# Kernel optimization log

Hardware: AMD Instinct MI355X
Metric: run time of the kernel (lower is better)

Reference implementation:

```python
import jax, jax.numpy as jnp
import numpy as np

# ---- static config (from module __init__ defaults) ----
INPUT_DIM = 3
NUM_LEVELS = 16
LEVEL_DIM = 2
SCALE = 2.0
BASE_RES = 16
LOG2_T = 19
MAX_T = 2 ** LOG2_T
NUM_FREQS = 6
N_POINTS = 2_000_000
PRIMES = np.array([1, 2654435761, 805459861], dtype=np.uint32)  # Instant-NGP spatial hash primes
CORNERS = np.array([[i, j, k] for i in (0, 1) for j in (0, 1) for k in (0, 1)], dtype=np.int32)  # [8,3]

RES = [int(np.floor(BASE_RES * SCALE ** l)) for l in range(NUM_LEVELS)]
SIZES = [min(MAX_T, (r + 1) ** 3) for r in RES]  # dense if the full grid fits in the hashmap
OFFSETS = np.concatenate([[0], np.cumsum(SIZES)]).astype(np.int64)
TOTAL = int(OFFSETS[-1])  # 7,131,219 rows


def setup_inputs() -> dict:
    key = jax.random.key(0)
    k1, k2 = jax.random.split(key)
    x = jax.random.uniform(k1, (N_POINTS, INPUT_DIM), dtype=jnp.float32)  # points in [0,1]^3
    # hash-grid features init U(-1e-4, 1e-4) as in Instant-NGP
    table = (jax.random.uniform(k2, (TOTAL, LEVEL_DIM), dtype=jnp.float32) * 2.0 - 1.0) * 1e-4
    return {"x": x, "table": table}


def _level_interp(x, table_l, res, size):
    """Trilinear hash-grid interpolation at one level. x:[N,3] in [0,1]."""
    pos = x * jnp.float32(res)            # [N,3]
    p0f = jnp.floor(pos)
    frac = pos - p0f                      # [N,3]
    p0 = p0f.astype(jnp.int32)
    corners = jnp.clip(p0[:, None, :] + CORNERS[None], 0, res)  # [N,8,3], grid has res+1 verts
    if (res + 1) ** 3 <= MAX_T:
        # dense stride indexing
        r1 = res + 1
        idx = corners[..., 0] + corners[..., 1] * r1 + corners[..., 2] * (r1 * r1)
    else:
        c = corners.astype(jnp.uint32)
        h = (c[..., 0] * jnp.uint32(int(PRIMES[0]))
             ^ c[..., 1] * jnp.uint32(int(PRIMES[1]))
             ^ c[..., 2] * jnp.uint32(int(PRIMES[2])))
        idx = (h % jnp.uint32(size)).astype(jnp.int32)
    vals = table_l[idx]                   # [N,8,level_dim] gather
    # trilinear weights: prod over dims of (frac if corner==1 else 1-frac)
    w = jnp.where(CORNERS[None] == 1, frac[:, None, :], 1.0 - frac[:, None, :]).prod(-1)  # [N,8]
    return jnp.einsum('nc,ncd->nd', w, vals)  # [N,level_dim]


def _hash_encode(x, table):
    feats = [
        _level_interp(x, table[int(OFFSETS[l]):int(OFFSETS[l + 1])], RES[l], SIZES[l])
        for l in range(NUM_LEVELS)
    ]
    return jnp.concatenate(feats, axis=-1)  # [N, num_levels*level_dim]


def _pos_encode(x):
    coeffs = jnp.float32(2.0) ** jnp.arange(NUM_FREQS, dtype=jnp.float32)  # log_sampling
    xc = x[:, None, :] * coeffs[None, :, None]           # [N,F,3]
    sc = jnp.stack([jnp.sin(xc), jnp.cos(xc)], axis=2)   # [N,F,2,3] -> order: per-freq sin(3) then cos(3)
    return jnp.concatenate([x, sc.reshape(x.shape[0], 2 * NUM_FREQS * INPUT_DIM)], axis=-1)


def reference(x, table):
    hash_feat = _hash_encode(x, table)   # [N,32]
    freq_feat = _pos_encode(x)           # [N,39]
    return jnp.concatenate([hash_feat, freq_feat], axis=-1)  # [N,71]
```

## Files before the change

kernel.cpp:

```cpp
#include <hip/hip_runtime.h>

typedef float f4 __attribute__((ext_vector_type(4)));

#define BLK 128
#define NLEV 16
#define NHASH 13
#define HSIZE 524288
#define HMASK 524287u
#define KOFF3 315475
#define CONV_BLOCKS ((NHASH * HSIZE) / 256)

__constant__ int kOff[NLEV] = {0, 4913, 40850, 315475, 839763, 1364051, 1888339,
                               2412627, 2936915, 3461203, 3985491, 4509779,
                               5034067, 5558355, 6082643, 6606931};

__global__ __launch_bounds__(256)
void prep_kernel(const float* __restrict__ xs, const float2* __restrict__ tab,
                 unsigned* __restrict__ tbf, f4* __restrict__ xs4, int n)
{
    const int b = blockIdx.x;
    if (b < CONV_BLOCKS) {
        const int i = b * 256 + threadIdx.x;
        float2 v = tab[KOFF3 + i];
        tbf[i] = (__float_as_uint(v.x) >> 16) | (__float_as_uint(v.y) & 0xFFFF0000u);
    } else {
        const int i = (b - CONV_BLOCKS) * 256 + threadIdx.x;
        if (i < n) {
            f4 p;
            p.x = xs[3 * i + 0];
            p.y = xs[3 * i + 1];
            p.z = xs[3 * i + 2];
            p.w = 0.f;
            __builtin_nontemporal_store(p, &xs4[i]);
        }
    }
}

__global__ __launch_bounds__(256)
void levels_kernel(const f4* __restrict__ xs4, const unsigned* __restrict__ tbf,
                   unsigned* __restrict__ scratch, int n)
{
    const int lev = blockIdx.y;
    const int i0  = blockIdx.x * 512 + threadIdx.x;
    const int res = 16 << (3 + lev);
    const float fres = (float)res;
    const unsigned* __restrict__ tl = tbf + (size_t)lev * HSIZE;

    unsigned hx[2], hc[2][4];
    float rx[2], ry[2], rz[2];
    bool valid[2];

    #pragma unroll
    for (int p = 0; p < 2; ++p) {
        const int i = i0 + p * 256;
        valid[p] = (i < n);
        f4 pt = {0.f, 0.f, 0.f, 0.f};
        if (valid[p]) pt = __builtin_nontemporal_load(&xs4[i]);
        float posx = pt.x * fres, posy = pt.y * fres, posz = pt.z * fres;
        float fxf = floorf(posx), fyf = floorf(posy), fzf = floorf(posz);
        rx[p] = posx - fxf; ry[p] = posy - fyf; rz[p] = posz - fzf;
        unsigned x  = (unsigned)(int)fxf;
        unsigned y0 = (unsigned)(int)fyf * 2654435761u, y1 = y0 + 2654435761u;
        unsigned z0 = (unsigned)(int)fzf * 805459861u,  z1 = z0 + 805459861u;
        hx[p] = x;
        hc[p][0] = y0 ^ z0; hc[p][1] = y0 ^ z1; hc[p][2] = y1 ^ z0; hc[p][3] = y1 ^ z1;
    }

    unsigned va[2][4], vb[2][4];
    #pragma unroll
    for (int p = 0; p < 2; ++p) {
        #pragma unroll
        for (int c = 0; c < 4; ++c) {
            unsigned ia = (hx[p] ^ hc[p][c]) & HMASK;
            uint2 q = *(const uint2*)(tl + (ia & ~1u));
            va[p][c] = (ia & 1u) ? q.y : q.x;
            vb[p][c] = (ia & 1u) ? q.x : q.y;
        }
    }
    #pragma unroll
    for (int p = 0; p < 2; ++p) {
        if (hx[p] & 1u) {
            unsigned x1 = hx[p] + 1u;
            #pragma unroll
            for (int c = 0; c < 4; ++c)
                vb[p][c] = tl[(x1 ^ hc[p][c]) & HMASK];
        }
    }

    #pragma unroll
    for (int p = 0; p < 2; ++p) {
        if (!valid[p]) continue;
        float wx1 = rx[p], wx0 = 1.f - wx1;
        float wy1 = ry[p], wy0 = 1.f - wy1;
        float wz1 = rz[p], wz0 = 1.f - wz1;
        float wc[4] = {wy0 * wz0, wy0 * wz1, wy1 * wz0, wy1 * wz1};
        float f0 = 0.f, f1 = 0.f;
        #pragma unroll
        for (int c = 0; c < 4; ++c) {
            float a0 = __uint_as_float(va[p][c] << 16);
            float a1 = __uint_as_float(va[p][c] & 0xFFFF0000u);
            float b0 = __uint_as_float(vb[p][c] << 16);
            float b1 = __uint_as_float(vb[p][c] & 0xFFFF0000u);
            f0 += wc[c] * (wx0 * a0 + wx1 * b0);
            f1 += wc[c] * (wx0 * a1 + wx1 * b1);
        }
        unsigned packed = (__float_as_uint(f0) >> 16) | (__float_as_uint(f1) & 0xFFFF0000u);
        __builtin_nontemporal_store(packed, &scratch[(size_t)lev * n + (i0 + p * 256)]);
    }
}

__global__ __launch_bounds__(256)
void levels_f32_kernel(const float* __restrict__ xs, const float2* __restrict__ tab,
                       unsigned* __restrict__ scratch, int n)
{
    const int lev = blockIdx.y;
    const int i   = blockIdx.x * 256 + threadIdx.x;
    if (i >= n) return;
    const int res = 16 << (3 + lev);
    const float2* __restrict__ tl = tab + kOff[3 + lev];

    const float px = __builtin_nontemporal_load(&xs[3 * i + 0]);
    const float py = __builtin_nontemporal_load(&xs[3 * i + 1]);
    const float pz = __builtin_nontemporal_load(&xs[3 * i + 2]);

    const float fres = (float)res;
    float posx = px * fres, posy = py * fres, posz = pz * fres;
    float fxf = floorf(posx), fyf = floorf(posy), fzf = floorf(posz);
    float rx = posx - fxf, ry = posy - fyf, rz = posz - fzf;

    unsigned hx  = (unsigned)(int)fxf;
    unsigned hy0 = (unsigned)(int)fyf * 2654435761u, hy1 = hy0 + 2654435761u;
    unsigned hz0 = (unsigned)(int)fzf * 805459861u,  hz1 = hz0 + 805459861u;
    unsigned h00 = hy0 ^ hz0, h01 = hy0 ^ hz1, h10 = hy1 ^ hz0, h11 = hy1 ^ hz1;

    unsigned hx1 = hx + 1u;
    float2 v000 = tl[(hx ^ h00) & HMASK], v100 = tl[(hx1 ^ h00) & HMASK];
    float2 v001 = tl[(hx ^ h01) & HMASK], v101 = tl[(hx1 ^ h01) & HMASK];
    float2 v010 = tl[(hx ^ h10) & HMASK], v110 = tl[(hx1 ^ h10) & HMASK];
    float2 v011 = tl[(hx ^ h11) & HMASK], v111 = tl[(hx1 ^ h11) & HMASK];

    float wx1 = rx, wx0 = 1.f - rx;
    float wy1 = ry, wy0 = 1.f - ry;
    float wz1 = rz, wz0 = 1.f - rz;

    float f0, f1, w;
    w = wx0 * wy0 * wz0; f0  = w * v000.x; f1  = w * v000.y;
    w = wx0 * wy0 * wz1; f0 += w * v001.x; f1 += w * v001.y;
    w = wx0 * wy1 * wz0; f0 += w * v010.x; f1 += w * v010.y;
    w = wx0 * wy1 * wz1; f0 += w * v011.x; f1 += w * v011.y;
    w = wx1 * wy0 * wz0; f0 += w * v100.x; f1 += w * v100.y;
    w = wx1 * wy0 * wz1; f0 += w * v101.x; f1 += w * v101.y;
    w = wx1 * wy1 * wz0; f0 += w * v110.x; f1 += w * v110.y;
    w = wx1 * wy1 * wz1; f0 += w * v111.x; f1 += w * v111.y;

    unsigned packed = (__float_as_uint(f0) >> 16) | (__float_as_uint(f1) & 0xFFFF0000u);
    __builtin_nontemporal_store(packed, &scratch[(size_t)lev * n + i]);
}

__global__ __launch_bounds__(BLK)
void final_kernel(const f4* __restrict__ xs4, const float* __restrict__ table,
                  const unsigned* __restrict__ scratch, float* __restrict__ out, int n)
{
    __shared__ float sbuf[BLK * 71];
    const int tid  = threadIdx.x;
    const int base = blockIdx.x * BLK;
    const int pi   = base + tid;
    const bool val = (pi < n);

    unsigned sc[NHASH];
    if (val) {
        #pragma unroll
        for (int h = 0; h < NHASH; ++h)
            sc[h] = __builtin_nontemporal_load(&scratch[(size_t)h * n + pi]);
    }

    f4 pt = {0.f, 0.f, 0.f, 0.f};
    if (val) pt = __builtin_nontemporal_load(&xs4[pi]);
    const float px = pt.x, py = pt.y, pz = pt.z;

    float* srow = sbuf + tid * 71;
    const float2* __restrict__ tab = (const float2*)table;

    #pragma unroll
    for (int l = 0; l < 3; ++l) {
        const int res = 16 << l;
        const float2* __restrict__ tl = tab + kOff[l];
        const float fres = (float)res;

        float posx = px * fres, posy = py * fres, posz = pz * fres;
        float fxf = floorf(posx), fyf = floorf(posy), fzf = floorf(posz);
        float rx = posx - fxf, ry = posy - fyf, rz = posz - fzf;

        const unsigned r1 = (unsigned)(res + 1);
        const unsigned r2 = r1 * r1;
        unsigned x0 = (unsigned)(int)fxf;
        unsigned by0 = (unsigned)(int)fyf * r1; unsigned by1 = by0 + r1;
        unsigned cz0 = (unsigned)(int)fzf * r2; unsigned cz1 = cz0 + r2;

        float2 v000, v001, v010, v011, v100, v101, v110, v111;
        #define PAIRD(B, VA, VB) { \
            unsigned i0 = x0 + (B); \
            if ((i0 & 1u) == 0u) { f4 q = *(const f4*)(tl + i0); \
                VA.x = q.x; VA.y = q.y; VB.x = q.z; VB.y = q.w; } \
            else { VA = tl[i0]; VB = tl[i0 + 1u]; } }
        PAIRD(by0 + cz0, v000, v100)
        PAIRD(by0 + cz1, v001, v101)
        PAIRD(by1 + cz0, v010, v110)
        PAIRD(by1 + cz1, v011, v111)
        #undef PAIRD

        float wx1 = rx, wx0 = 1.f - rx;
        float wy1 = ry, wy0 = 1.f - ry;
        float wz1 = rz, wz0 = 1.f - rz;

        float f0, f1, w;
        w = wx0 * wy0 * wz0; f0  = w * v000.x; f1  = w * v000.y;
        w = wx0 * wy0 * wz1; f0 += w * v001.x; f1 += w * v001.y;
        w = wx0 * wy1 * wz0; f0 += w * v010.x; f1 += w * v010.y;
        w = wx0 * wy1 * wz1; f0 += w * v011.x; f1 += w * v011.y;
        w = wx1 * wy0 * wz0; f0 += w * v100.x; f1 += w * v100.y;
        w = wx1 * wy0 * wz1; f0 += w * v101.x; f1 += w * v101.y;
        w = wx1 * wy1 * wz0; f0 += w * v110.x; f1 += w * v110.y;
        w = wx1 * wy1 * wz1; f0 += w * v111.x; f1 += w * v111.y;

        srow[2 * l]     = f0;
        srow[2 * l + 1] = f1;
    }

    #pragma unroll
    for (int h = 0; h < NHASH; ++h) {
        srow[6 + 2 * h] = __uint_as_float(sc[h] << 16);
        srow[7 + 2 * h] = __uint_as_float(sc[h] & 0xFFFF0000u);
    }

    srow[32] = px; srow[33] = py; srow[34] = pz;
    float sx, cx, sy, cy, sz, cz;
    __sincosf(px, &sx, &cx);
    __sincosf(py, &sy, &cy);
    __sincosf(pz, &sz, &cz);
    #pragma unroll
    for (int f = 0; f < 6; ++f) {
        srow[35 + 6*f + 0] = sx; srow[35 + 6*f + 3] = cx;
        srow[35 + 6*f + 1] = sy; srow[35 + 6*f + 4] = cy;
        srow[35 + 6*f + 2] = sz; srow[35 + 6*f + 5] = cz;
        if (f < 5) {
            float nsx = 2.f * sx * cx, ncx = 1.f - 2.f * sx * sx;
            float nsy = 2.f * sy * cy, ncy = 1.f - 2.f * sy * sy;
            float nsz = 2.f * sz * cz, ncz = 1.f - 2.f * sz * sz;
            sx = nsx; cx = ncx; sy = nsy; cy = ncy; sz = nsz; cz = ncz;
        }
    }

    __syncthreads();

    const int nvalid = min(BLK, n - base);
    float* obase = out + (size_t)base * 71;
    if (nvalid == BLK) {
        f4* o4 = (f4*)obase;
        const f4* s4 = (const f4*)sbuf;
        #pragma unroll 1
        for (int i = tid; i < (BLK * 71) / 4; i += BLK)
            __builtin_nontemporal_store(s4[i], &o4[i]);
    } else {
        #pragma unroll 1
        for (int i = tid; i < nvalid * 71; i += BLK)
            __builtin_nontemporal_store(sbuf[i], &obase[i]);
    }
}

__global__ __launch_bounds__(BLK)
void final_f32_kernel(const float* __restrict__ xs, const float* __restrict__ table,
                      const unsigned* __restrict__ scratch, float* __restrict__ out, int n)
{
    __shared__ float sbuf[BLK * 71];
    const int tid  = threadIdx.x;
    const int base = blockIdx.x * BLK;
    const int pi   = base + tid;

    float px = 0.f, py = 0.f, pz = 0.f;
    if (pi < n) { px = xs[3*pi]; py = xs[3*pi+1]; pz = xs[3*pi+2]; }

    float* srow = sbuf + tid * 71;
    const float2* __restrict__ tab = (const float2*)table;

    #pragma unroll
    for (int l = 0; l < 3; ++l) {
        const int res = 16 << l;
        const float2* __restrict__ tl = tab + kOff[l];
        const float fres = (float)res;
        float posx = px * fres, posy = py * fres, posz = pz * fres;
        float fxf = floorf(posx), fyf = floorf(posy), fzf = floorf(posz);
        float rx = posx - fxf, ry = posy - fyf, rz = posz - fzf;
        const unsigned r1 = (unsigned)(res + 1), r2 = r1 * r1;
        unsigned x0 = (unsigned)(int)fxf;
        unsigned by0 = (unsigned)(int)fyf * r1, by1 = by0 + r1;
        unsigned cz0 = (unsigned)(int)fzf * r2, cz1 = cz0 + r2;
        float2 v000 = tl[x0+by0+cz0], v100 = tl[x0+by0+cz0+1];
        float2 v001 = tl[x0+by0+cz1], v101 = tl[x0+by0+cz1+1];
        float2 v010 = tl[x0+by1+cz0], v110 = tl[x0+by1+cz0+1];
        float2 v011 = tl[x0+by1+cz1], v111 = tl[x0+by1+cz1+1];
        float wx1 = rx, wx0 = 1.f - rx, wy1 = ry, wy0 = 1.f - ry, wz1 = rz, wz0 = 1.f - rz;
        float f0, f1, w;
        w = wx0*wy0*wz0; f0  = w*v000.x; f1  = w*v000.y;
        w = wx0*wy0*wz1; f0 += w*v001.x; f1 += w*v001.y;
        w = wx0*wy1*wz0; f0 += w*v010.x; f1 += w*v010.y;
        w = wx0*wy1*wz1; f0 += w*v011.x; f1 += w*v011.y;
        w = wx1*wy0*wz0; f0 += w*v100.x; f1 += w*v100.y;
        w = wx1*wy0*wz1; f0 += w*v101.x; f1 += w*v101.y;
        w = wx1*wy1*wz0; f0 += w*v110.x; f1 += w*v110.y;
        w = wx1*wy1*wz1; f0 += w*v111.x; f1 += w*v111.y;
        srow[2*l] = f0; srow[2*l+1] = f1;
    }
    if (pi < n) {
        #pragma unroll
        for (int h = 0; h < NHASH; ++h) {
            unsigned u = __builtin_nontemporal_load(&scratch[(size_t)h * n + pi]);
            srow[6+2*h] = __uint_as_float(u << 16);
            srow[7+2*h] = __uint_as_float(u & 0xFFFF0000u);
        }
    }
    srow[32] = px; srow[33] = py; srow[34] = pz;
    float coef = 1.f;
    #pragma unroll
    for (int f = 0; f < 6; ++f) {
        float s, c;
        __sincosf(px*coef, &s, &c); srow[35+6*f+0] = s; srow[35+6*f+3] = c;
        __sincosf(py*coef, &s, &c); srow[35+6*f+1] = s; srow[35+6*f+4] = c;
        __sincosf(pz*coef, &s, &c); srow[35+6*f+2] = s; srow[35+6*f+5] = c;
        coef *= 2.f;
    }
    __syncthreads();
    const int nvalid = min(BLK, n - base);
    float* obase = out + (size_t)base * 71;
    if (nvalid == BLK) {
        f4* o4 = (f4*)obase;
        const f4* s4 = (const f4*)sbuf;
        #pragma unroll 1
        for (int i = tid; i < (BLK * 71) / 4; i += BLK)
            __builtin_nontemporal_store(s4[i], &o4[i]);
    } else {
        #pragma unroll 1
        for (int i = tid; i < nvalid * 71; i += BLK)
            __builtin_nontemporal_store(sbuf[i], &obase[i]);
    }
}

extern "C" void kernel_launch(void* const* d_in, const int* in_sizes, int n_in,
                              void* d_out, int out_size, void* d_ws, size_t ws_size,
                              hipStream_t stream) {
    const float* xs    = (const float*)d_in[0];
    const float* table = (const float*)d_in[1];
    float* out = (float*)d_out;
    const int n = in_sizes[0] / 3;

    unsigned* scratch = (unsigned*)d_ws;
    const size_t featBytes = (size_t)NHASH * (size_t)n * 4u;
    const size_t tblBytes  = (size_t)NHASH * HSIZE * 4u;
    const size_t xs4Bytes  = (size_t)n * 16u;
    const float2* tab = (const float2*)table;
    const int gf = (n + BLK - 1) / BLK;

    if (ws_size >= featBytes + tblBytes + xs4Bytes) {
        unsigned* tbf = (unsigned*)((char*)d_ws + featBytes);
        f4* xs4 = (f4*)((char*)d_ws + featBytes + tblBytes);

        const int packBlocks = (n + 255) / 256;
        hipLaunchKernelGGL(prep_kernel, dim3(CONV_BLOCKS + packBlocks), dim3(256),
                           0, stream, xs, tab, tbf, xs4, n);

        const int bpl = (n + 511) / 512;
        hipLaunchKernelGGL(levels_kernel, dim3(bpl, NHASH), dim3(256), 0, stream,
                           xs4, tbf, scratch, n);
        hipLaunchKernelGGL(final_kernel, dim3(gf), dim3(BLK), 0, stream,
                           xs4, table, scratch, out, n);
    } else {
        const int bpl = (n + 255) / 256;
        hipLaunchKernelGGL(levels_f32_kernel, dim3(bpl, NHASH), dim3(256), 0, stream,
                           xs, tab, scratch, n);
        hipLaunchKernelGGL(final_f32_kernel, dim3(gf), dim3(BLK), 0, stream,
                           xs, table, scratch, out, n);
    }
}
```

Before: 897.3 us.

## Shrink LDS staging rows and compute sin/cos during the coalesced output write

The final kernels now stage only the 35 hash and raw-coordinate values per point in shared memory (row stride 36 instead of 71). The 36 positional-encoding values are computed on the fly inside the cooperative store loop with one sincos per element, using per-element integer div/mod to find the point and feature. This halves shared memory per block, which can raise occupancy, but replaces the cheap double-angle recurrence with direct sincos calls and adds index arithmetic and divergent branches in the store loop. The levels kernel's coordinate load also becomes an ordinary cached load instead of a nontemporal one.

New measurement: 882.4 us. No clear change (-1.7%).

```diff
diff --git a/kernel.cpp b/kernel.cpp
--- a/kernel.cpp
+++ b/kernel.cpp
@@ -8,6 +8,7 @@
 #define HSIZE 524288
 #define HMASK 524287u
 #define KOFF3 315475
+#define SROW 36
 #define CONV_BLOCKS ((NHASH * HSIZE) / 256)
 
 __constant__ int kOff[NLEV] = {0, 4913, 40850, 315475, 839763, 1364051, 1888339,
@@ -55,7 +56,7 @@
         const int i = i0 + p * 256;
         valid[p] = (i < n);
         f4 pt = {0.f, 0.f, 0.f, 0.f};
-        if (valid[p]) pt = __builtin_nontemporal_load(&xs4[i]);
+        if (valid[p]) pt = xs4[i];
         float posx = pt.x * fres, posy = pt.y * fres, posz = pt.z * fres;
         float fxf = floorf(posx), fyf = floorf(posy), fzf = floorf(posz);
         rx[p] = posx - fxf; ry[p] = posy - fyf; rz[p] = posz - fzf;
@@ -161,7 +162,7 @@
 void final_kernel(const f4* __restrict__ xs4, const float* __restrict__ table,
                   const unsigned* __restrict__ scratch, float* __restrict__ out, int n)
 {
-    __shared__ float sbuf[BLK * 71];
+    __shared__ float sbuf[BLK * SROW];
     const int tid  = threadIdx.x;
     const int base = blockIdx.x * BLK;
     const int pi   = base + tid;
@@ -178,7 +179,7 @@
     if (val) pt = __builtin_nontemporal_load(&xs4[pi]);
     const float px = pt.x, py = pt.y, pz = pt.z;
 
-    float* srow = sbuf + tid * 71;
+    float* srow = sbuf + tid * SROW;
     const float2* __restrict__ tab = (const float2*)table;
 
     #pragma unroll
@@ -232,24 +233,7 @@
         srow[6 + 2 * h] = __uint_as_float(sc[h] << 16);
         srow[7 + 2 * h] = __uint_as_float(sc[h] & 0xFFFF0000u);
     }
-
     srow[32] = px; srow[33] = py; srow[34] = pz;
-    float sx, cx, sy, cy, sz, cz;
-    __sincosf(px, &sx, &cx);
-    __sincosf(py, &sy, &cy);
-    __sincosf(pz, &sz, &cz);
-    #pragma unroll
-    for (int f = 0; f < 6; ++f) {
-        srow[35 + 6*f + 0] = sx; srow[35 + 6*f + 3] = cx;
-        srow[35 + 6*f + 1] = sy; srow[35 + 6*f + 4] = cy;
-        srow[35 + 6*f + 2] = sz; srow[35 + 6*f + 5] = cz;
-        if (f < 5) {
-            float nsx = 2.f * sx * cx, ncx = 1.f - 2.f * sx * sx;
-            float nsy = 2.f * sy * cy, ncy = 1.f - 2.f * sy * sy;
-            float nsz = 2.f * sz * cz, ncz = 1.f - 2.f * sz * sz;
-            sx = nsx; cx = ncx; sy = nsy; cy = ncy; sz = nsz; cz = ncz;
-        }
-    }
 
     __syncthreads();
 
@@ -257,14 +241,52 @@
     float* obase = out + (size_t)base * 71;
     if (nvalid == BLK) {
         f4* o4 = (f4*)obase;
-        const f4* s4 = (const f4*)sbuf;
         #pragma unroll 1
-        for (int i = tid; i < (BLK * 71) / 4; i += BLK)
-            __builtin_nontemporal_store(s4[i], &o4[i]);
+        for (int i = tid; i < (BLK * 71) / 4; i += BLK) {
+            const int e = 4 * i;
+            f4 v;
+            #pragma unroll
+            for (int j = 0; j < 4; ++j) {
+                const int ee = e + j;
+                const int p = ee / 71;
+                const int f = ee - p * 71;
+                float valf;
+                if (f < 35) {
+                    valf = sbuf[p * SROW + f];
+                } else {
+                    const int g = f - 35;
+                    const int freq = g / 6;
+                    const int r = g - 6 * freq;
+                    const int dim = (r < 3) ? r : r - 3;
+                    const float a = sbuf[p * SROW + 32 + dim] * (float)(1 << freq);
+                    float s, c;
+                    __sincosf(a, &s, &c);
+                    valf = (r < 3) ? s : c;
+                }
+                v[j] = valf;
+            }
+            __builtin_nontemporal_store(v, &o4[i]);
+        }
     } else {
         #pragma unroll 1
-        for (int i = tid; i < nvalid * 71; i += BLK)
-            __builtin_nontemporal_store(sbuf[i], &obase[i]);
+        for (int i = tid; i < nvalid * 71; i += BLK) {
+            const int p = i / 71;
+            const int f = i - p * 71;
+            float valf;
+            if (f < 35) {
+                valf = sbuf[p * SROW + f];
+            } else {
+                const int g = f - 35;
+                const int freq = g / 6;
+                const int r = g - 6 * freq;
+                const int dim = (r < 3) ? r : r - 3;
+                const float a = sbuf[p * SROW + 32 + dim] * (float)(1 << freq);
+                float s, c;
+                __sincosf(a, &s, &c);
+                valf = (r < 3) ? s : c;
+            }
+            __builtin_nontemporal_store(valf, &obase[i]);
+        }
     }
 }
 
@@ -272,7 +294,7 @@
 void final_f32_kernel(const float* __restrict__ xs, const float* __restrict__ table,
                       const unsigned* __restrict__ scratch, float* __restrict__ out, int n)
 {
-    __shared__ float sbuf[BLK * 71];
+    __shared__ float sbuf[BLK * SROW];
     const int tid  = threadIdx.x;
     const int base = blockIdx.x * BLK;
     const int pi   = base + tid;
@@ -280,7 +302,7 @@
     float px = 0.f, py = 0.f, pz = 0.f;
     if (pi < n) { px = xs[3*pi]; py = xs[3*pi+1]; pz = xs[3*pi+2]; }
 
-    float* srow = sbuf + tid * 71;
+    float* srow = sbuf + tid * SROW;
     const float2* __restrict__ tab = (const float2*)table;
 
     #pragma unroll
@@ -320,28 +342,27 @@
         }
     }
     srow[32] = px; srow[33] = py; srow[34] = pz;
-    float coef = 1.f;
-    #pragma unroll
-    for (int f = 0; f < 6; ++f) {
-        float s, c;
-        __sincosf(px*coef, &s, &c); srow[35+6*f+0] = s; srow[35+6*f+3] = c;
-        __sincosf(py*coef, &s, &c); srow[35+6*f+1] = s; srow[35+6*f+4] = c;
-        __sincosf(pz*coef, &s, &c); srow[35+6*f+2] = s; srow[35+6*f+5] = c;
-        coef *= 2.f;
-    }
     __syncthreads();
     const int nvalid = min(BLK, n - base);
     float* obase = out + (size_t)base * 71;
-    if (nvalid == BLK) {
-        f4* o4 = (f4*)obase;
-        const f4* s4 = (const f4*)sbuf;
-        #pragma unroll 1
-        for (int i = tid; i < (BLK * 71) / 4; i += BLK)
-            __builtin_nontemporal_store(s4[i], &o4[i]);
-    } else {
-        #pragma unroll 1
-        for (int i = tid; i < nvalid * 71; i += BLK)
-            __builtin_nontemporal_store(sbuf[i], &obase[i]);
+    #pragma unroll 1
+    for (int i = tid; i < nvalid * 71; i += BLK) {
+        const int p = i / 71;
+        const int f = i - p * 71;
+        float valf;
+        if (f < 35) {
+            valf = sbuf[p * SROW + f];
+        } else {
+            const int g = f - 35;
+            const int freq = g / 6;
+            const int r = g - 6 * freq;
+            const int dim = (r < 3) ? r : r - 3;
+            const float a = sbuf[p * SROW + 32 + dim] * (float)(1 << freq);
+            float s, c;
+            __sincosf(a, &s, &c);
+            valf = (r < 3) ? s : c;
+        }
+        __builtin_nontemporal_store(valf, &obase[i]);
     }
 }
 
```
